# Kernel tuning notes

Measured on AMD Instinct MI355X. Metric: run time of the kernel, lower is better.

## Reference

```python
import jax, jax.numpy as jnp
import numpy as np

I_, J_, D_IN, D_H = 100, 8, 768, 64
N_NODES, N_HE, N_INC, N_CELLS, VOCAB = 160000, 320000, 1600000, 800, 30000
BN_EPS = 1e-5


def setup_inputs() -> dict:
    key = jax.random.key(0)
    ks = jax.random.split(key, 20)
    w = lambda k, s: jax.random.normal(k, s, jnp.float32) * 0.05
    inp = {}
    inp['x'] = jax.random.normal(ks[0], (I_, J_, D_IN), jnp.float32)
    inp['node_tokens'] = jax.random.randint(ks[1], (N_NODES,), 0, VOCAB)
    inp['inc_node'] = jax.random.randint(ks[2], (N_INC,), 0, N_NODES)
    inp['inc_hedge'] = jnp.sort(jax.random.randint(ks[3], (N_INC,), 0, N_HE))
    inp['node2cell'] = jnp.sort(jax.random.randint(ks[4], (N_NODES,), 0, N_CELLS))
    inp['vac_emb'] = w(ks[5], (VOCAB, D_IN))
    inp['fhi_w'] = w(ks[6], (D_IN, D_H)); inp['fhi_b'] = jnp.zeros((D_H,), jnp.float32)
    inp['fin_w'] = w(ks[7], (D_IN, D_H)); inp['fin_b'] = jnp.zeros((D_H,), jnp.float32)
    inp['th1'] = w(ks[8], (D_H, D_H)); inp['b1'] = jnp.zeros((D_H,), jnp.float32)
    inp['th2'] = w(ks[9], (D_H, D_H)); inp['b2'] = jnp.zeros((D_H,), jnp.float32)
    for li, k in zip((1, 2, 3), (ks[10], ks[11], ks[12])):
        inp[f'wc{li}'] = w(k, (D_H, D_H, 3))
        inp[f'bc{li}'] = jnp.zeros((D_H,), jnp.float32)
        inp[f'g{li}'] = jnp.ones((D_H,), jnp.float32)
        inp[f'be{li}'] = jnp.zeros((D_H,), jnp.float32)
        inp[f'm{li}'] = jnp.zeros((D_H,), jnp.float32)
        inp[f'v{li}'] = jnp.ones((D_H,), jnp.float32)
    inp['fct_w'] = w(ks[13], (D_H, D_H)); inp['fct_b'] = jnp.zeros((D_H,), jnp.float32)
    return inp


def _inv_safe(c):
    return jnp.where(c > 0, 1.0 / jnp.maximum(c, 1.0), 0.0)


def _hconv(xf, inc_node, inc_hedge, theta, bias):
    # PyG HypergraphConv (no attention): D^{-1} H W B^{-1} H^T (X Theta) + bias
    xt = xf @ theta                                        # [N, D]
    ones = jnp.ones((inc_node.shape[0],), xt.dtype)
    deg_e = jax.ops.segment_sum(ones, inc_hedge, N_HE)     # B_e
    he = jax.ops.segment_sum(xt[inc_node], inc_hedge, N_HE) * _inv_safe(deg_e)[:, None]
    deg_v = jax.ops.segment_sum(ones, inc_node, N_NODES)   # D_v
    out = jax.ops.segment_sum(he[inc_hedge], inc_node, N_NODES) * _inv_safe(deg_v)[:, None]
    return out + bias


def _conv_bn(h, wc, bc, g, be, m, v):
    # Conv1d(k=3, pad=1) -> ReLU -> BatchNorm1d (inference stats); dropout is eval-mode identity
    h = jax.lax.conv_general_dilated(h, wc, (1,), [(1, 1)],
                                     dimension_numbers=('NCH', 'OIH', 'NCH')) + bc[None, :, None]
    h = jax.nn.relu(h)
    return (h - m[None, :, None]) * (g[None, :, None] / jnp.sqrt(v[None, :, None] + BN_EPS)) + be[None, :, None]


def _forward(x, node_tokens, inc_node, inc_hedge, node2cell, vac_emb, fhi_w, fhi_b,
             fin_w, fin_b, th1, b1, th2, b2, wc1, bc1, g1, be1, m1, v1,
             wc2, bc2, g2, be2, m2, v2, wc3, bc3, g3, be3, m3, v3, fct_w, fct_b):
    # x = fin(x)
    x0 = jnp.einsum('ijd,dh->ijh', x, fin_w) + fin_b       # [100, 8, 64]
    # node_features = fhi(graph_embedding[graph.x])  (gather-dominated)
    nf = vac_emb[node_tokens] @ fhi_w + fhi_b              # [N, 64]
    # two HypergraphConv layers with residuals (eval-mode dropout = identity)
    h1 = jax.nn.relu(_hconv(nf, inc_node, inc_hedge, th1, b1)) + nf
    gx = jax.nn.relu(_hconv(h1, inc_node, inc_hedge, th2, b2)) + nf
    # per-graph mean + max pooling (graph.batch is all-zero per graph => one vector per cell)
    cnt = jax.ops.segment_sum(jnp.ones((N_NODES,), gx.dtype), node2cell, N_CELLS)
    mean_p = jax.ops.segment_sum(gx, node2cell, N_CELLS) * _inv_safe(cnt)[:, None]
    max_p = jax.ops.segment_max(gx, node2cell, N_CELLS)
    max_p = jnp.where(cnt[:, None] > 0, max_p, 0.0)
    cell_emb = 0.5 * (mean_p + max_p)                      # [800, 64]
    x_upd = x0 + 0.3 * cell_emb.reshape(I_, J_, D_H)       # x[i,j] += 0.3*graph_emb
    h = jnp.transpose(x_upd, (0, 2, 1))                    # [100, 64, 8]
    h = _conv_bn(h, wc1, bc1, g1, be1, m1, v1)
    h = _conv_bn(h, wc2, bc2, g2, be2, m2, v2)
    h = _conv_bn(h, wc3, bc3, g3, be3, m3, v3)
    out2 = jnp.mean(h, axis=2) @ fct_w + fct_b             # [100, 64]
    return x_upd, out2


def reference(x, node_tokens, inc_node, inc_hedge, node2cell, vac_emb, fhi_w, fhi_b,
              fin_w, fin_b, th1, b1, th2, b2, wc1, bc1, g1, be1, m1, v1,
              wc2, bc2, g2, be2, m2, v2, wc3, bc3, g3, be3, m3, v3, fct_w, fct_b):
    return _forward(x, node_tokens, inc_node, inc_hedge, node2cell, vac_emb, fhi_w, fhi_b,
                    fin_w, fin_b, th1, b1, th2, b2, wc1, bc1, g1, be1, m1, v1,
                    wc2, bc2, g2, be2, m2, v2, wc3, bc3, g3, be3, m3, v3, fct_w, fct_b)
```

## Files before the change

### kernel.cpp

```cpp
#include <hip/hip_runtime.h>
#include <hip/hip_bf16.h>
#include <cstdint>
#include <cstddef>

#define I_      100
#define J_      8
#define D_IN    768
#define D_H     64
#define N_NODES 160000
#define N_HE    320000
#define N_INC   1600000
#define N_CELLS 800
#define VOCAB   30000

#define NRANGE   256
#define NPR      625
#define EPB      (N_INC / 256)
#define SLAB     8192

typedef unsigned short u16;
using short8 = __attribute__((ext_vector_type(8))) short;
using f32x4  = __attribute__((ext_vector_type(4))) float;

__device__ __forceinline__ float bf2f(u16 u) {
    union { uint32_t i; float f; } x; x.i = ((uint32_t)u) << 16; return x.f;
}
__device__ __forceinline__ u16 f2bf(float f) {
    union { float f; uint32_t i; } x; x.f = f;
    uint32_t b = x.i;
    b += 0x7FFFu + ((b >> 16) & 1u);
    return (u16)(b >> 16);
}
__device__ __forceinline__ float lo_bf(uint32_t u) {
    union { uint32_t i; float f; } x; x.i = u << 16; return x.f;
}
__device__ __forceinline__ float hi_bf(uint32_t u) {
    union { uint32_t i; float f; } x; x.i = u & 0xFFFF0000u; return x.f;
}
__device__ __forceinline__ uint32_t pack_bf2(float a, float b) {
    return (uint32_t)f2bf(a) | ((uint32_t)f2bf(b) << 16);
}

#define G_OFF_HE   (N_INC / 256)
#define G_OFF_CELL (N_NODES / 256)
#define G_CONV_BIG ((D_IN * 64) / 256)
#define G_CONV_SM  ((64 * 64) / 256)
#define G_KA       256
#define G_KB1      256
#define G_KC       256
#define G_KD       256
#define G_PGEMM    ((VOCAB + 63) / 64)
#define G_XT       (N_NODES / 64)
#define G_X0       ((I_ * J_ + 63) / 64)
#define G_HEDGE    (N_HE / 32)
#define G_NODE     (N_NODES / 32)

__device__ __forceinline__ void dev_offsets(int bid, const int* __restrict__ sorted,
                                            int n, int nbins, int* __restrict__ off) {
    int i = bid * 256 + threadIdx.x;
    if (i >= n) return;
    int cur = sorted[i];
    int prev = (i == 0) ? -1 : sorted[i - 1];
    for (int b = prev + 1; b <= cur; ++b) off[b] = i;
    if (i == n - 1) {
        for (int b = cur + 1; b <= nbins; ++b) off[b] = n;
    }
}

__device__ __forceinline__ void dev_convT(int bid, const float* __restrict__ B,
                                          u16* __restrict__ Bt, int K) {
    int g = bid * 256 + threadIdx.x;
    if (g >= K * 64) return;
    int k = g >> 6, n = g & 63;
    Bt[(size_t)n * K + k] = f2bf(B[g]);
}

__device__ __forceinline__ void dev_ka(int bid, const int* __restrict__ inc_node,
                                       int* __restrict__ counts, int* __restrict__ lds) {
    int tid = threadIdx.x;
    lds[tid] = 0;
    __syncthreads();
    int s = bid * EPB, e = s + EPB;
    for (int i = s + tid; i < e; i += 256)
        atomicAdd(&lds[(unsigned)inc_node[i] / NPR], 1);
    __syncthreads();
    counts[bid * NRANGE + tid] = lds[tid];
}

__device__ __forceinline__ void dev_kb1(int r, const int* __restrict__ counts,
                                        int* __restrict__ chunk_off,
                                        int* __restrict__ range_total,
                                        int* __restrict__ lds) {
    int b = threadIdx.x;
    int v = counts[b * NRANGE + r];
    lds[b] = v;
    __syncthreads();
    #pragma unroll
    for (int d = 1; d < 256; d <<= 1) {
        int t = (b >= d) ? lds[b - d] : 0;
        __syncthreads();
        lds[b] += t;
        __syncthreads();
    }
    int incl = lds[b];
    chunk_off[b * NRANGE + r] = incl - v;
    if (b == 255) range_total[r] = incl;
}

__device__ __forceinline__ void dev_kc(int bid, const int* __restrict__ inc_node,
                                       const int* __restrict__ inc_hedge,
                                       const int* __restrict__ chunk_off,
                                       int2* __restrict__ bucket, int* __restrict__ lds) {
    int tid = threadIdx.x;
    int* co  = lds;
    int* cur = lds + 256;
    co[tid]  = tid * SLAB + chunk_off[bid * NRANGE + tid];
    cur[tid] = 0;
    __syncthreads();
    int s = bid * EPB, e = s + EPB;
    for (int i = s + tid; i < e; i += 256) {
        int v = inc_node[i];
        int h = inc_hedge[i];
        int rg = (unsigned)v / NPR;
        int rank = atomicAdd(&cur[rg], 1);
        bucket[co[rg] + rank] = make_int2(v, h);
    }
}

__device__ __forceinline__ void dev_kd(int r, const int2* __restrict__ bucket,
                                       const int* __restrict__ range_total,
                                       int* __restrict__ node_off, int* __restrict__ node_deg,
                                       int* __restrict__ csr, int* __restrict__ lds) {
    int tid = threadIdx.x;
    int* hist = lds;
    int* tsum = lds + 768;
    int* cur  = lds + 1024;
    for (int i = tid; i < 768; i += 256) { hist[i] = 0; cur[i] = 0; }
    __syncthreads();
    int lo = r * NPR;
    int pb = r * SLAB;
    int pe = pb + range_total[r];
    for (int i = pb + tid; i < pe; i += 256)
        atomicAdd(&hist[bucket[i].x - lo], 1);
    __syncthreads();
    int b3 = tid * 3;
    int a0 = hist[b3], a1 = hist[b3 + 1], a2 = hist[b3 + 2];
    int s = a0 + a1 + a2;
    tsum[tid] = s;
    __syncthreads();
    #pragma unroll
    for (int d = 1; d < 256; d <<= 1) {
        int t = (tid >= d) ? tsum[tid - d] : 0;
        __syncthreads();
        tsum[tid] += t;
        __syncthreads();
    }
    int excl = tsum[tid] - s;
    hist[b3]     = excl;
    hist[b3 + 1] = excl + a0;
    hist[b3 + 2] = excl + a0 + a1;
    __syncthreads();
    for (int v = tid; v < NPR; v += 256) {
        int h0 = hist[v];
        node_off[lo + v] = pb + h0;
        node_deg[lo + v] = hist[v + 1] - h0;
    }
    for (int i = pb + tid; i < pe; i += 256) {
        int2 p = bucket[i];
        int l = p.x - lo;
        int k = atomicAdd(&cur[l], 1);
        csr[pb + hist[l] + k] = p.y;
    }
}

template <int BF16_OUT, int GATHER, int KK>
__device__ __forceinline__ void dev_gemm_direct(int wid, const float* __restrict__ A,
                                                const int* __restrict__ tok,
                                                const u16* __restrict__ Bt,
                                                const float* __restrict__ bias,
                                                void* __restrict__ C, int M) {
    int lane = threadIdx.x & 63;
    int m16 = lane & 15, q = lane >> 4;
    int base = wid << 4;
    if (base >= M) return;
    int row = base + m16;
    const float* arow = GATHER ? (A + ((size_t)tok[row] << 6))
                               : (A + (size_t)row * KK);

    f32x4 acc0 = {0.f, 0.f, 0.f, 0.f};
    f32x4 acc1 = {0.f, 0.f, 0.f, 0.f};
    f32x4 acc2 = {0.f, 0.f, 0.f, 0.f};
    f32x4 acc3 = {0.f, 0.f, 0.f, 0.f};

    #pragma unroll 2
    for (int kt = 0; kt < KK; kt += 32) {
        const float* ap = arow + kt + q * 8;
        float4 av0 = *reinterpret_cast<const float4*>(ap);
        float4 av1 = *reinterpret_cast<const float4*>(ap + 4);
        short8 a;
        a[0] = (short)f2bf(av0.x); a[1] = (short)f2bf(av0.y);
        a[2] = (short)f2bf(av0.z); a[3] = (short)f2bf(av0.w);
        a[4] = (short)f2bf(av1.x); a[5] = (short)f2bf(av1.y);
        a[6] = (short)f2bf(av1.z); a[7] = (short)f2bf(av1.w);
        const u16* bp = Bt + (size_t)m16 * KK + kt + q * 8;
        short8 b0 = *reinterpret_cast<const short8*>(bp);
        short8 b1 = *reinterpret_cast<const short8*>(bp + (size_t)16 * KK);
        short8 b2 = *reinterpret_cast<const short8*>(bp + (size_t)32 * KK);
        short8 b3 = *reinterpret_cast<const short8*>(bp + (size_t)48 * KK);
        acc0 = __builtin_amdgcn_mfma_f32_16x16x32_bf16(a, b0, acc0, 0, 0, 0);
        acc1 = __builtin_amdgcn_mfma_f32_16x16x32_bf16(a, b1, acc1, 0, 0, 0);
        acc2 = __builtin_amdgcn_mfma_f32_16x16x32_bf16(a, b2, acc2, 0, 0, 0);
        acc3 = __builtin_amdgcn_mfma_f32_16x16x32_bf16(a, b3, acc3, 0, 0, 0);
    }

    f32x4 accs[4] = {acc0, acc1, acc2, acc3};
    #pragma unroll
    for (int r = 0; r < 4; ++r) {
        int gr = base + q * 4 + r;
        #pragma unroll
        for (int j = 0; j < 4; ++j) {
            int col = j * 16 + m16;
            float v = accs[j][r];
            if (!BF16_OUT) v += bias[col];
            if (BF16_OUT)
                ((u16*)C)[(size_t)gr * 64 + col] = f2bf(v);
            else
                ((float*)C)[(size_t)gr * 64 + col] = v;
        }
    }
}

__device__ __forceinline__ void dev_hedge_sum(int bid, const int* __restrict__ inc_node,
                                              const int* __restrict__ he_off,
                                              const u16* __restrict__ xt,
                                              u16* __restrict__ he) {
    int w = (bid * 256 + (int)threadIdx.x) >> 6;
    int lane = threadIdx.x & 63;
    int sub = lane >> 3;
    int c8 = (lane & 7) << 3;
    int hedge = w * 8 + sub;
    if (hedge >= N_HE) return;
    int s = he_off[hedge], e = he_off[hedge + 1];

    float a0 = 0.f, a1 = 0.f, a2 = 0.f, a3 = 0.f;
    float a4 = 0.f, a5 = 0.f, a6 = 0.f, a7 = 0.f;
    float b0 = 0.f, b1 = 0.f, b2 = 0.f, b3 = 0.f;
    float b4 = 0.f, b5 = 0.f, b6 = 0.f, b7 = 0.f;

    int j = s;
    if ((e - s) & 1) {
        uint4 d = *reinterpret_cast<const uint4*>(xt + (((size_t)inc_node[j]) << 6) + c8);
        a0 += lo_bf(d.x); a1 += hi_bf(d.x);
        a2 += lo_bf(d.y); a3 += hi_bf(d.y);
        a4 += lo_bf(d.z); a5 += hi_bf(d.z);
        a6 += lo_bf(d.w); a7 += hi_bf(d.w);
        ++j;
    }
    int i0 = 0, i1 = 0;
    if (j < e) { i0 = inc_node[j]; i1 = inc_node[j + 1]; }
    for (; j < e; j += 2) {
        int c0 = i0, c1 = i1;
        if (j + 2 < e) { i0 = inc_node[j + 2]; i1 = inc_node[j + 3]; }
        uint4 d0 = *reinterpret_cast<const uint4*>(xt + (((size_t)c0) << 6) + c8);
        uint4 d1 = *reinterpret_cast<const uint4*>(xt + (((size_t)c1) << 6) + c8);
        a0 += lo_bf(d0.x); a1 += hi_bf(d0.x);
        a2 += lo_bf(d0.y); a3 += hi_bf(d0.y);
        a4 += lo_bf(d0.z); a5 += hi_bf(d0.z);
        a6 += lo_bf(d0.w); a7 += hi_bf(d0.w);
        b0 += lo_bf(d1.x); b1 += hi_bf(d1.x);
        b2 += lo_bf(d1.y); b3 += hi_bf(d1.y);
        b4 += lo_bf(d1.z); b5 += hi_bf(d1.z);
        b6 += lo_bf(d1.w); b7 += hi_bf(d1.w);
    }
    a0 += b0; a1 += b1; a2 += b2; a3 += b3;
    a4 += b4; a5 += b5; a6 += b6; a7 += b7;

    float inv = (e > s) ? 1.f / (float)(e - s) : 0.f;
    uint4 o;
    o.x = pack_bf2(a0 * inv, a1 * inv);
    o.y = pack_bf2(a2 * inv, a3 * inv);
    o.z = pack_bf2(a4 * inv, a5 * inv);
    o.w = pack_bf2(a6 * inv, a7 * inv);
    *reinterpret_cast<uint4*>(he + (((size_t)hedge) << 6) + c8) = o;
}

__device__ __forceinline__ void dev_node_sum(int bid, const int* __restrict__ csr,
                                             const int* __restrict__ node_off,
                                             const int* __restrict__ node_deg,
                                             const u16* __restrict__ he,
                                             const float* __restrict__ bias,
                                             const float* __restrict__ P,
                                             const int* __restrict__ tok,
                                             float* __restrict__ out) {
    int w = (bid * 256 + (int)threadIdx.x) >> 6;
    int lane = threadIdx.x & 63;
    int sub = lane >> 3;
    int c8 = (lane & 7) << 3;
    int node = w * 8 + sub;
    if (node >= N_NODES) return;
    int s = node_off[node];
    int e = s + node_deg[node];

    float a0 = 0.f, a1 = 0.f, a2 = 0.f, a3 = 0.f;
    float a4 = 0.f, a5 = 0.f, a6 = 0.f, a7 = 0.f;
    float b0 = 0.f, b1 = 0.f, b2 = 0.f, b3 = 0.f;
    float b4 = 0.f, b5 = 0.f, b6 = 0.f, b7 = 0.f;

    int j = s;
    if ((e - s) & 1) {
        uint4 d = *reinterpret_cast<const uint4*>(he + (((size_t)csr[j]) << 6) + c8);
        a0 += lo_bf(d.x); a1 += hi_bf(d.x);
        a2 += lo_bf(d.y); a3 += hi_bf(d.y);
        a4 += lo_bf(d.z); a5 += hi_bf(d.z);
        a6 += lo_bf(d.w); a7 += hi_bf(d.w);
        ++j;
    }
    int i0 = 0, i1 = 0;
    if (j < e) { i0 = csr[j]; i1 = csr[j + 1]; }
    for (; j < e; j += 2) {
        int c0 = i0, c1 = i1;
        if (j + 2 < e) { i0 = csr[j + 2]; i1 = csr[j + 3]; }
        uint4 d0 = *reinterpret_cast<const uint4*>(he + (((size_t)c0) << 6) + c8);
        uint4 d1 = *reinterpret_cast<const uint4*>(he + (((size_t)c1) << 6) + c8);
        a0 += lo_bf(d0.x); a1 += hi_bf(d0.x);
        a2 += lo_bf(d0.y); a3 += hi_bf(d0.y);
        a4 += lo_bf(d0.z); a5 += hi_bf(d0.z);
        a6 += lo_bf(d0.w); a7 += hi_bf(d0.w);
        b0 += lo_bf(d1.x); b1 += hi_bf(d1.x);
        b2 += lo_bf(d1.y); b3 += hi_bf(d1.y);
        b4 += lo_bf(d1.z); b5 += hi_bf(d1.z);
        b6 += lo_bf(d1.w); b7 += hi_bf(d1.w);
    }
    a0 += b0; a1 += b1; a2 += b2; a3 += b3;
    a4 += b4; a5 += b5; a6 += b6; a7 += b7;

    float inv = (e > s) ? 1.f / (float)(e - s) : 0.f;
    const float* nfp = P + (((size_t)tok[node]) << 6) + c8;
    float4 nv0 = *reinterpret_cast<const float4*>(nfp);
    float4 nv1 = *reinterpret_cast<const float4*>(nfp + 4);
    float4 o0, o1;
    o0.x = fmaxf(fmaf(a0, inv, bias[c8 + 0]), 0.f) + nv0.x;
    o0.y = fmaxf(fmaf(a1, inv, bias[c8 + 1]), 0.f) + nv0.y;
    o0.z = fmaxf(fmaf(a2, inv, bias[c8 + 2]), 0.f) + nv0.z;
    o0.w = fmaxf(fmaf(a3, inv, bias[c8 + 3]), 0.f) + nv0.w;
    o1.x = fmaxf(fmaf(a4, inv, bias[c8 + 4]), 0.f) + nv1.x;
    o1.y = fmaxf(fmaf(a5, inv, bias[c8 + 5]), 0.f) + nv1.y;
    o1.z = fmaxf(fmaf(a6, inv, bias[c8 + 6]), 0.f) + nv1.z;
    o1.w = fmaxf(fmaf(a7, inv, bias[c8 + 7]), 0.f) + nv1.w;
    float* op = out + (((size_t)node) << 6) + c8;
    *reinterpret_cast<float4*>(op) = o0;
    *reinterpret_cast<float4*>(op + 4) = o1;
}

__global__ __launch_bounds__(256) void k_p0(const float* __restrict__ fhi_w,
                                            const float* __restrict__ fin_w,
                                            const float* __restrict__ th1,
                                            const float* __restrict__ th2,
                                            u16* __restrict__ Bt_fhi, u16* __restrict__ Bt_fin,
                                            u16* __restrict__ Bt_th1, u16* __restrict__ Bt_th2,
                                            const int* __restrict__ inc_node,
                                            int* __restrict__ counts) {
    __shared__ int lds[256];
    int bid = blockIdx.x;
    if (bid < G_KA) { dev_ka(bid, inc_node, counts, lds); return; }
    bid -= G_KA;
    if (bid < G_CONV_BIG) { dev_convT(bid, fhi_w, Bt_fhi, D_IN); return; }
    bid -= G_CONV_BIG;
    if (bid < G_CONV_BIG) { dev_convT(bid, fin_w, Bt_fin, D_IN); return; }
    bid -= G_CONV_BIG;
    if (bid < G_CONV_SM) { dev_convT(bid, th1, Bt_th1, 64); return; }
    bid -= G_CONV_SM;
    dev_convT(bid, th2, Bt_th2, 64);
}

__global__ __launch_bounds__(256) void k_p1(const float* __restrict__ vac_emb,
                                            const u16* __restrict__ Bt_fhi,
                                            const float* __restrict__ fhi_b, float* __restrict__ P,
                                            const int* __restrict__ counts,
                                            int* __restrict__ chunk_off, int* __restrict__ range_total,
                                            const int* __restrict__ inc_hedge,
                                            const int* __restrict__ node2cell,
                                            int* __restrict__ he_off, int* __restrict__ cell_off) {
    __shared__ int lds[256];
    int bid = blockIdx.x;
    if (bid < G_PGEMM) {
        int wid = bid * 4 + ((int)threadIdx.x >> 6);
        dev_gemm_direct<0, 0, D_IN>(wid, vac_emb, nullptr, Bt_fhi, fhi_b, P, VOCAB);
        return;
    }
    bid -= G_PGEMM;
    if (bid < G_KB1) { dev_kb1(bid, counts, chunk_off, range_total, lds); return; }
    bid -= G_KB1;
    if (bid < G_OFF_HE) { dev_offsets(bid, inc_hedge, N_INC, N_HE, he_off); return; }
    bid -= G_OFF_HE;
    dev_offsets(bid, node2cell, N_NODES, N_CELLS, cell_off);
}

__global__ __launch_bounds__(256) void k_p2(const float* __restrict__ P,
                                            const int* __restrict__ tok,
                                            const u16* __restrict__ Bt_th1, u16* __restrict__ xt,
                                            const float* __restrict__ x, const u16* __restrict__ Bt_fin,
                                            const float* __restrict__ fin_b, float* __restrict__ x0,
                                            const int* __restrict__ inc_node,
                                            const int* __restrict__ inc_hedge,
                                            const int* __restrict__ chunk_off,
                                            int2* __restrict__ bucket) {
    __shared__ int lds[512];
    int bid = blockIdx.x;
    if (bid < G_XT) {
        int wid = bid * 4 + ((int)threadIdx.x >> 6);
        dev_gemm_direct<1, 1, 64>(wid, P, tok, Bt_th1, nullptr, xt, N_NODES);
        return;
    }
    bid -= G_XT;
    if (bid < G_KC) { dev_kc(bid, inc_node, inc_hedge, chunk_off, bucket, lds); return; }
    bid -= G_KC;
    {
        int wid = bid * 4 + ((int)threadIdx.x >> 6);
        dev_gemm_direct<0, 0, D_IN>(wid, x, nullptr, Bt_fin, fin_b, x0, I_ * J_);
    }
}

__global__ __launch_bounds__(256) void k_p3(const int* __restrict__ inc_node,
                                            const int* __restrict__ he_off,
                                            const u16* __restrict__ xt, u16* __restrict__ he,
                                            const int2* __restrict__ bucket,
                                            const int* __restrict__ range_total,
                                            int* __restrict__ node_off, int* __restrict__ node_deg,
                                            int* __restrict__ csr) {
    __shared__ int lds[1792];
    int bid = blockIdx.x;
    if (bid < G_HEDGE) { dev_hedge_sum(bid, inc_node, he_off, xt, he); return; }
    bid -= G_HEDGE;
    dev_kd(bid, bucket, range_total, node_off, node_deg, csr, lds);
}

__global__ __launch_bounds__(256) void k_xt2(const float* __restrict__ A,
                                             const u16* __restrict__ Bt,
                                             u16* __restrict__ xt) {
    int wid = blockIdx.x * 4 + ((int)threadIdx.x >> 6);
    dev_gemm_direct<1, 0, 64>(wid, A, nullptr, Bt, nullptr, xt, N_NODES);
}

__global__ __launch_bounds__(256) void k_hedge_sum(const int* __restrict__ inc_node,
                                                   const int* __restrict__ he_off,
                                                   const u16* __restrict__ xt,
                                                   u16* __restrict__ he) {
    dev_hedge_sum(blockIdx.x, inc_node, he_off, xt, he);
}

__global__ __launch_bounds__(256) void k_node_sum(const int* __restrict__ csr,
                                                  const int* __restrict__ node_off,
                                                  const int* __restrict__ node_deg,
                                                  const u16* __restrict__ he,
                                                  const float* __restrict__ bias,
                                                  const float* __restrict__ P,
                                                  const int* __restrict__ tok,
                                                  float* __restrict__ out) {
    dev_node_sum(blockIdx.x, csr, node_off, node_deg, he, bias, P, tok, out);
}

__global__ __launch_bounds__(256) void k_pool(const float* __restrict__ gx,
                                              const int* __restrict__ cell_off,
                                              const float* __restrict__ x0,
                                              float* __restrict__ out1) {
    __shared__ float ssum[4][64];
    __shared__ float smax[4][64];
    int c = blockIdx.x;
    int lane = threadIdx.x & 63;
    int w = threadIdx.x >> 6;
    int s = cell_off[c], e = cell_off[c + 1];
    float sum = 0.f, mx = -INFINITY;
    for (int n = s + w; n < e; n += 4) {
        float v = gx[((size_t)n << 6) + lane];
        sum += v;
        mx = fmaxf(mx, v);
    }
    ssum[w][lane] = sum;
    smax[w][lane] = mx;
    __syncthreads();
    if (w == 0) {
        sum = ssum[0][lane] + ssum[1][lane] + ssum[2][lane] + ssum[3][lane];
        mx = fmaxf(fmaxf(smax[0][lane], smax[1][lane]), fmaxf(smax[2][lane], smax[3][lane]));
        int cnt = e - s;
        float mean = (cnt > 0) ? sum / (float)cnt : 0.f;
        float mp = (cnt > 0) ? mx : 0.f;
        float ce = 0.5f * (mean + mp);
        out1[((size_t)c << 6) + lane] = x0[((size_t)c << 6) + lane] + 0.3f * ce;
    }
}

__global__ __launch_bounds__(256) void k_tcn(
    const float* __restrict__ xu,
    const float* __restrict__ wc1, const float* __restrict__ bc1, const float* __restrict__ g1,
    const float* __restrict__ be1, const float* __restrict__ m1, const float* __restrict__ v1,
    const float* __restrict__ wc2, const float* __restrict__ bc2, const float* __restrict__ g2,
    const float* __restrict__ be2, const float* __restrict__ m2, const float* __restrict__ v2,
    const float* __restrict__ wc3, const float* __restrict__ bc3, const float* __restrict__ g3,
    const float* __restrict__ be3, const float* __restrict__ m3, const float* __restrict__ v3,
    const float* __restrict__ fct_w, const float* __restrict__ fct_b,
    float* __restrict__ out2) {
    __shared__ float w_lds[64 * 64 * 3];
    __shared__ float hA[64][10];
    __shared__ float hB[64][10];
    __shared__ float mo[64];

    int n = blockIdx.x, tid = threadIdx.x;

    if (tid < 64) {
        hA[tid][0] = 0.f; hA[tid][9] = 0.f;
        hB[tid][0] = 0.f; hB[tid][9] = 0.f;
    }
    #pragma unroll
    for (int l = tid; l < 512; l += 256) {
        int t = l >> 6, i = l & 63;
        hA[i][t + 1] = xu[(size_t)n * 512 + l];
    }

    const float* wcs[3] = {wc1, wc2, wc3};
    const float* bcs[3] = {bc1, bc2, bc3};
    const float* gs[3]  = {g1, g2, g3};
    const float* bes[3] = {be1, be2, be3};
    const float* ms[3]  = {m1, m2, m3};
    const float* vs[3]  = {v1, v2, v3};

    float (*hin)[10] = hA;
    float (*hout)[10] = hB;

    #pragma unroll
    for (int li = 0; li < 3; ++li) {
        for (int l = tid; l < 64 * 64 * 3; l += 256) w_lds[l] = wcs[li][l];
        __syncthreads();
        #pragma unroll
        for (int rep = 0; rep < 2; ++rep) {
            int idx = tid + rep * 256;
            int o = idx >> 3, t = idx & 7;
            float acc = bcs[li][o];
            #pragma unroll 8
            for (int i = 0; i < 64; ++i) {
                const float* wr = &w_lds[o * 192 + i * 3];
                acc = fmaf(hin[i][t + 0], wr[0], acc);
                acc = fmaf(hin[i][t + 1], wr[1], acc);
                acc = fmaf(hin[i][t + 2], wr[2], acc);
            }
            acc = fmaxf(acc, 0.f);
            float sc = gs[li][o] * rsqrtf(vs[li][o] + 1e-5f);
            acc = (acc - ms[li][o]) * sc + bes[li][o];
            hout[o][t + 1] = acc;
        }
        __syncthreads();
        float (*tmp)[10] = hin; hin = hout; hout = tmp;
    }

    if (tid < 64) {
        float s = 0.f;
        #pragma unroll
        for (int t = 0; t < 8; ++t) s += hin[tid][t + 1];
        mo[tid] = s * 0.125f;
    }
    __syncthreads();
    if (tid < 64) {
        float acc = fct_b[tid];
        #pragma unroll 8
        for (int o = 0; o < 64; ++o) acc = fmaf(mo[o], fct_w[o * 64 + tid], acc);
        out2[(size_t)n * 64 + tid] = acc;
    }
}

extern "C" void kernel_launch(void* const* d_in, const int* in_sizes, int n_in,
                              void* d_out, int out_size, void* d_ws, size_t ws_size,
                              hipStream_t stream) {
    (void)in_sizes; (void)n_in; (void)out_size; (void)ws_size;

    const float* x          = (const float*)d_in[0];
    const int*   node_tok   = (const int*)d_in[1];
    const int*   inc_node   = (const int*)d_in[2];
    const int*   inc_hedge  = (const int*)d_in[3];
    const int*   node2cell  = (const int*)d_in[4];
    const float* vac_emb    = (const float*)d_in[5];
    const float* fhi_w      = (const float*)d_in[6];
    const float* fhi_b      = (const float*)d_in[7];
    const float* fin_w      = (const float*)d_in[8];
    const float* fin_b      = (const float*)d_in[9];
    const float* th1        = (const float*)d_in[10];
    const float* b1         = (const float*)d_in[11];
    const float* th2        = (const float*)d_in[12];
    const float* b2         = (const float*)d_in[13];
    const float* fct_w      = (const float*)d_in[32];
    const float* fct_b      = (const float*)d_in[33];

    char* ws = (char*)d_ws;
    size_t off = 0;
    float* P        = (float*)(ws + off); off += (size_t)VOCAB * 64 * 4;
    float* hbuf     = (float*)(ws + off); off += (size_t)N_NODES * 64 * 4;
    u16*   xt       = (u16*)(ws + off);   off += (size_t)N_NODES * 64 * 2;
    u16*   he       = (u16*)(ws + off);   off += (size_t)N_HE * 64 * 2;
    int2*  bucket   = (int2*)(ws + off);  off += (size_t)NRANGE * SLAB * 8;
    int*   csr      = (int*)(ws + off);   off += (size_t)NRANGE * SLAB * 4;
    float* x0       = (float*)(ws + off); off += (size_t)N_CELLS * 64 * 4;
    u16*   Bt_fhi   = (u16*)(ws + off);   off += (size_t)64 * D_IN * 2;
    u16*   Bt_fin   = (u16*)(ws + off);   off += (size_t)64 * D_IN * 2;
    u16*   Bt_th1   = (u16*)(ws + off);   off += (size_t)64 * 64 * 2;
    u16*   Bt_th2   = (u16*)(ws + off);   off += (size_t)64 * 64 * 2;
    int*   he_off   = (int*)(ws + off);   off += ((size_t)(N_HE + 1) * 4 + 255) / 256 * 256;
    int*   node_off = (int*)(ws + off);   off += (size_t)N_NODES * 4;
    int*   node_deg = (int*)(ws + off);   off += (size_t)N_NODES * 4;
    int*   cell_off = (int*)(ws + off);   off += ((size_t)(N_CELLS + 1) * 4 + 255) / 256 * 256;

    int*  counts      = (int*)hbuf;
    int*  chunk_off   = counts + NRANGE * NRANGE;
    int*  range_total = chunk_off + NRANGE * NRANGE;

    float* out1 = (float*)d_out;
    float* out2 = out1 + (size_t)I_ * J_ * D_H;

    k_p0<<<G_KA + 2 * G_CONV_BIG + 2 * G_CONV_SM, 256, 0, stream>>>(
        fhi_w, fin_w, th1, th2, Bt_fhi, Bt_fin, Bt_th1, Bt_th2, inc_node, counts);

    k_p1<<<G_PGEMM + G_KB1 + G_OFF_HE + G_OFF_CELL, 256, 0, stream>>>(
        vac_emb, Bt_fhi, fhi_b, P, counts, chunk_off, range_total,
        inc_hedge, node2cell, he_off, cell_off);

    k_p2<<<G_XT + G_KC + G_X0, 256, 0, stream>>>(P, node_tok, Bt_th1, xt,
                                                 x, Bt_fin, fin_b, x0,
                                                 inc_node, inc_hedge, chunk_off, bucket);

    k_p3<<<G_HEDGE + G_KD, 256, 0, stream>>>(inc_node, he_off, xt, he,
                                             bucket, range_total, node_off, node_deg, csr);

    k_node_sum<<<G_NODE, 256, 0, stream>>>(csr, node_off, node_deg, he, b1, P, node_tok, hbuf);

    k_xt2<<<G_XT, 256, 0, stream>>>(hbuf, Bt_th2, xt);

    k_hedge_sum<<<G_HEDGE, 256, 0, stream>>>(inc_node, he_off, xt, he);

    k_node_sum<<<G_NODE, 256, 0, stream>>>(csr, node_off, node_deg, he, b2, P, node_tok, hbuf);

    k_pool<<<N_CELLS, 256, 0, stream>>>(hbuf, cell_off, x0, out1);

    k_tcn<<<I_, 256, 0, stream>>>(out1,
        (const float*)d_in[14], (const float*)d_in[15], (const float*)d_in[16],
        (const float*)d_in[17], (const float*)d_in[18], (const float*)d_in[19],
        (const float*)d_in[20], (const float*)d_in[21], (const float*)d_in[22],
        (const float*)d_in[23], (const float*)d_in[24], (const float*)d_in[25],
        (const float*)d_in[26], (const float*)d_in[27], (const float*)d_in[28],
        (const float*)d_in[29], (const float*)d_in[30], (const float*)d_in[31],
        fct_w, fct_b, out2);
}
```

Before: 514.7 us.

## Build node CSR with global atomics instead of two-pass range bucketing

Replaces the four-stage range-bucketed counting sort (per-chunk LDS histograms, cross-chunk scan, bucket scatter, per-range local sort) with direct global atomic degree counting, a per-range scan to produce node offsets, and an atomic-cursor scatter straight into the CSR. This removes the intermediate int2 bucket buffer and one full pass over the incidences. In exchange it relies on contended global atomics over random node indices and adds zeroing of two node-sized arrays. Within-node edge order becomes nondeterministic, which can change float summation order.

```diff
diff --git a/kernel.cpp b/kernel.cpp
--- a/kernel.cpp
+++ b/kernel.cpp
@@ -15,7 +15,6 @@
 
 #define NRANGE   256
 #define NPR      625
-#define EPB      (N_INC / 256)
 #define SLAB     8192
 
 typedef unsigned short u16;
@@ -45,10 +44,10 @@
 #define G_OFF_CELL (N_NODES / 256)
 #define G_CONV_BIG ((D_IN * 64) / 256)
 #define G_CONV_SM  ((64 * 64) / 256)
-#define G_KA       256
-#define G_KB1      256
-#define G_KC       256
-#define G_KD       256
+#define G_ZD4      ((N_NODES / 4 + 255) / 256)
+#define G_KAH      512
+#define G_KBS      256
+#define G_KCS      512
 #define G_PGEMM    ((VOCAB + 63) / 64)
 #define G_XT       (N_NODES / 64)
 #define G_X0       ((I_ * J_ + 63) / 64)
@@ -75,101 +74,54 @@
     Bt[(size_t)n * K + k] = f2bf(B[g]);
 }
 
-__device__ __forceinline__ void dev_ka(int bid, const int* __restrict__ inc_node,
-                                       int* __restrict__ counts, int* __restrict__ lds) {
+__device__ __forceinline__ void dev_zero4(int bid, int* __restrict__ p, int n4) {
+    int g = bid * 256 + threadIdx.x;
+    if (g < n4) reinterpret_cast<int4*>(p)[g] = make_int4(0, 0, 0, 0);
+}
+
+__device__ __forceinline__ void dev_kah(int bid, const int* __restrict__ inc_node,
+                                        int* __restrict__ node_deg) {
+    int s = bid * (N_INC / G_KAH);
+    int e = s + (N_INC / G_KAH);
+    for (int i = s + (int)threadIdx.x; i < e; i += 256)
+        atomicAdd(&node_deg[inc_node[i]], 1);
+}
+
+__device__ __forceinline__ void dev_kbs(int r, const int* __restrict__ node_deg,
+                                        int* __restrict__ node_off, int* __restrict__ lds) {
     int tid = threadIdx.x;
-    lds[tid] = 0;
-    __syncthreads();
-    int s = bid * EPB, e = s + EPB;
-    for (int i = s + tid; i < e; i += 256)
-        atomicAdd(&lds[(unsigned)inc_node[i] / NPR], 1);
-    __syncthreads();
-    counts[bid * NRANGE + tid] = lds[tid];
-}
-
-__device__ __forceinline__ void dev_kb1(int r, const int* __restrict__ counts,
-                                        int* __restrict__ chunk_off,
-                                        int* __restrict__ range_total,
-                                        int* __restrict__ lds) {
-    int b = threadIdx.x;
-    int v = counts[b * NRANGE + r];
-    lds[b] = v;
+    int lo = r * NPR, pb = r * SLAB;
+    int v0 = tid * 3;
+    int d0 = (v0     < NPR) ? node_deg[lo + v0]     : 0;
+    int d1 = (v0 + 1 < NPR) ? node_deg[lo + v0 + 1] : 0;
+    int d2 = (v0 + 2 < NPR) ? node_deg[lo + v0 + 2] : 0;
+    int s = d0 + d1 + d2;
+    lds[tid] = s;
     __syncthreads();
     #pragma unroll
     for (int d = 1; d < 256; d <<= 1) {
-        int t = (b >= d) ? lds[b - d] : 0;
+        int t = (tid >= d) ? lds[tid - d] : 0;
         __syncthreads();
-        lds[b] += t;
+        lds[tid] += t;
         __syncthreads();
     }
-    int incl = lds[b];
-    chunk_off[b * NRANGE + r] = incl - v;
-    if (b == 255) range_total[r] = incl;
-}
-
-__device__ __forceinline__ void dev_kc(int bid, const int* __restrict__ inc_node,
-                                       const int* __restrict__ inc_hedge,
-                                       const int* __restrict__ chunk_off,
-                                       int2* __restrict__ bucket, int* __restrict__ lds) {
-    int tid = threadIdx.x;
-    int* co  = lds;
-    int* cur = lds + 256;
-    co[tid]  = tid * SLAB + chunk_off[bid * NRANGE + tid];
-    cur[tid] = 0;
-    __syncthreads();
-    int s = bid * EPB, e = s + EPB;
-    for (int i = s + tid; i < e; i += 256) {
+    int excl = lds[tid] - s;
+    if (v0     < NPR) node_off[lo + v0]     = pb + excl;
+    if (v0 + 1 < NPR) node_off[lo + v0 + 1] = pb + excl + d0;
+    if (v0 + 2 < NPR) node_off[lo + v0 + 2] = pb + excl + d0 + d1;
+}
+
+__device__ __forceinline__ void dev_kcs(int bid, const int* __restrict__ inc_node,
+                                        const int* __restrict__ inc_hedge,
+                                        const int* __restrict__ node_off,
+                                        int* __restrict__ cur, int* __restrict__ csr) {
+    int s = bid * (N_INC / G_KCS);
+    int e = s + (N_INC / G_KCS);
+    for (int i = s + (int)threadIdx.x; i < e; i += 256) {
         int v = inc_node[i];
         int h = inc_hedge[i];
-        int rg = (unsigned)v / NPR;
-        int rank = atomicAdd(&cur[rg], 1);
-        bucket[co[rg] + rank] = make_int2(v, h);
-    }
-}
-
-__device__ __forceinline__ void dev_kd(int r, const int2* __restrict__ bucket,
-                                       const int* __restrict__ range_total,
-                                       int* __restrict__ node_off, int* __restrict__ node_deg,
-                                       int* __restrict__ csr, int* __restrict__ lds) {
-    int tid = threadIdx.x;
-    int* hist = lds;
-    int* tsum = lds + 768;
-    int* cur  = lds + 1024;
-    for (int i = tid; i < 768; i += 256) { hist[i] = 0; cur[i] = 0; }
-    __syncthreads();
-    int lo = r * NPR;
-    int pb = r * SLAB;
-    int pe = pb + range_total[r];
-    for (int i = pb + tid; i < pe; i += 256)
-        atomicAdd(&hist[bucket[i].x - lo], 1);
-    __syncthreads();
-    int b3 = tid * 3;
-    int a0 = hist[b3], a1 = hist[b3 + 1], a2 = hist[b3 + 2];
-    int s = a0 + a1 + a2;
-    tsum[tid] = s;
-    __syncthreads();
-    #pragma unroll
-    for (int d = 1; d < 256; d <<= 1) {
-        int t = (tid >= d) ? tsum[tid - d] : 0;
-        __syncthreads();
-        tsum[tid] += t;
-        __syncthreads();
-    }
-    int excl = tsum[tid] - s;
-    hist[b3]     = excl;
-    hist[b3 + 1] = excl + a0;
-    hist[b3 + 2] = excl + a0 + a1;
-    __syncthreads();
-    for (int v = tid; v < NPR; v += 256) {
-        int h0 = hist[v];
-        node_off[lo + v] = pb + h0;
-        node_deg[lo + v] = hist[v + 1] - h0;
-    }
-    for (int i = pb + tid; i < pe; i += 256) {
-        int2 p = bucket[i];
-        int l = p.x - lo;
-        int k = atomicAdd(&cur[l], 1);
-        csr[pb + hist[l] + k] = p.y;
+        int k = atomicAdd(&cur[v], 1);
+        csr[node_off[v] + k] = h;
     }
 }
 
@@ -358,12 +310,12 @@
                                             const float* __restrict__ th2,
                                             u16* __restrict__ Bt_fhi, u16* __restrict__ Bt_fin,
                                             u16* __restrict__ Bt_th1, u16* __restrict__ Bt_th2,
-                                            const int* __restrict__ inc_node,
-                                            int* __restrict__ counts) {
-    __shared__ int lds[256];
+                                            int* __restrict__ node_deg, int* __restrict__ cur) {
     int bid = blockIdx.x;
-    if (bid < G_KA) { dev_ka(bid, inc_node, counts, lds); return; }
-    bid -= G_KA;
+    if (bid < G_ZD4) { dev_zero4(bid, node_deg, N_NODES / 4); return; }
+    bid -= G_ZD4;
+    if (bid < G_ZD4) { dev_zero4(bid, cur, N_NODES / 4); return; }
+    bid -= G_ZD4;
     if (bid < G_CONV_BIG) { dev_convT(bid, fhi_w, Bt_fhi, D_IN); return; }
     bid -= G_CONV_BIG;
     if (bid < G_CONV_BIG) { dev_convT(bid, fin_w, Bt_fin, D_IN); return; }
@@ -376,12 +328,11 @@
 __global__ __launch_bounds__(256) void k_p1(const float* __restrict__ vac_emb,
                                             const u16* __restrict__ Bt_fhi,
                                             const float* __restrict__ fhi_b, float* __restrict__ P,
-                                            const int* __restrict__ counts,
-                                            int* __restrict__ chunk_off, int* __restrict__ range_total,
+                                            const int* __restrict__ inc_node,
+                                            int* __restrict__ node_deg,
                                             const int* __restrict__ inc_hedge,
                                             const int* __restrict__ node2cell,
                                             int* __restrict__ he_off, int* __restrict__ cell_off) {
-    __shared__ int lds[256];
     int bid = blockIdx.x;
     if (bid < G_PGEMM) {
         int wid = bid * 4 + ((int)threadIdx.x >> 6);
@@ -389,8 +340,8 @@
         return;
     }
     bid -= G_PGEMM;
-    if (bid < G_KB1) { dev_kb1(bid, counts, chunk_off, range_total, lds); return; }
-    bid -= G_KB1;
+    if (bid < G_KAH) { dev_kah(bid, inc_node, node_deg); return; }
+    bid -= G_KAH;
     if (bid < G_OFF_HE) { dev_offsets(bid, inc_hedge, N_INC, N_HE, he_off); return; }
     bid -= G_OFF_HE;
     dev_offsets(bid, node2cell, N_NODES, N_CELLS, cell_off);
@@ -401,20 +352,18 @@
                                             const u16* __restrict__ Bt_th1, u16* __restrict__ xt,
                                             const float* __restrict__ x, const u16* __restrict__ Bt_fin,
                                             const float* __restrict__ fin_b, float* __restrict__ x0,
-                                            const int* __restrict__ inc_node,
-                                            const int* __restrict__ inc_hedge,
-                                            const int* __restrict__ chunk_off,
-                                            int2* __restrict__ bucket) {
-    __shared__ int lds[512];
+                                            const int* __restrict__ node_deg,
+                                            int* __restrict__ node_off) {
+    __shared__ int lds[256];
     int bid = blockIdx.x;
+    if (bid < G_KBS) { dev_kbs(bid, node_deg, node_off, lds); return; }
+    bid -= G_KBS;
     if (bid < G_XT) {
         int wid = bid * 4 + ((int)threadIdx.x >> 6);
         dev_gemm_direct<1, 1, 64>(wid, P, tok, Bt_th1, nullptr, xt, N_NODES);
         return;
     }
     bid -= G_XT;
-    if (bid < G_KC) { dev_kc(bid, inc_node, inc_hedge, chunk_off, bucket, lds); return; }
-    bid -= G_KC;
     {
         int wid = bid * 4 + ((int)threadIdx.x >> 6);
         dev_gemm_direct<0, 0, D_IN>(wid, x, nullptr, Bt_fin, fin_b, x0, I_ * J_);
@@ -424,15 +373,13 @@
 __global__ __launch_bounds__(256) void k_p3(const int* __restrict__ inc_node,
                                             const int* __restrict__ he_off,
                                             const u16* __restrict__ xt, u16* __restrict__ he,
-                                            const int2* __restrict__ bucket,
-                                            const int* __restrict__ range_total,
-                                            int* __restrict__ node_off, int* __restrict__ node_deg,
-                                            int* __restrict__ csr) {
-    __shared__ int lds[1792];
+                                            const int* __restrict__ inc_hedge,
+                                            const int* __restrict__ node_off,
+                                            int* __restrict__ cur, int* __restrict__ csr) {
     int bid = blockIdx.x;
-    if (bid < G_HEDGE) { dev_hedge_sum(bid, inc_node, he_off, xt, he); return; }
-    bid -= G_HEDGE;
-    dev_kd(bid, bucket, range_total, node_off, node_deg, csr, lds);
+    if (bid < G_KCS) { dev_kcs(bid, inc_node, inc_hedge, node_off, cur, csr); return; }
+    bid -= G_KCS;
+    dev_hedge_sum(bid, inc_node, he_off, xt, he);
 }
 
 __global__ __launch_bounds__(256) void k_xt2(const float* __restrict__ A,
@@ -595,7 +542,6 @@
     float* hbuf     = (float*)(ws + off); off += (size_t)N_NODES * 64 * 4;
     u16*   xt       = (u16*)(ws + off);   off += (size_t)N_NODES * 64 * 2;
     u16*   he       = (u16*)(ws + off);   off += (size_t)N_HE * 64 * 2;
-    int2*  bucket   = (int2*)(ws + off);  off += (size_t)NRANGE * SLAB * 8;
     int*   csr      = (int*)(ws + off);   off += (size_t)NRANGE * SLAB * 4;
     float* x0       = (float*)(ws + off); off += (size_t)N_CELLS * 64 * 4;
     u16*   Bt_fhi   = (u16*)(ws + off);   off += (size_t)64 * D_IN * 2;
@@ -605,28 +551,25 @@
     int*   he_off   = (int*)(ws + off);   off += ((size_t)(N_HE + 1) * 4 + 255) / 256 * 256;
     int*   node_off = (int*)(ws + off);   off += (size_t)N_NODES * 4;
     int*   node_deg = (int*)(ws + off);   off += (size_t)N_NODES * 4;
+    int*   cur      = (int*)(ws + off);   off += (size_t)N_NODES * 4;
     int*   cell_off = (int*)(ws + off);   off += ((size_t)(N_CELLS + 1) * 4 + 255) / 256 * 256;
-
-    int*  counts      = (int*)hbuf;
-    int*  chunk_off   = counts + NRANGE * NRANGE;
-    int*  range_total = chunk_off + NRANGE * NRANGE;
 
     float* out1 = (float*)d_out;
     float* out2 = out1 + (size_t)I_ * J_ * D_H;
 
-    k_p0<<<G_KA + 2 * G_CONV_BIG + 2 * G_CONV_SM, 256, 0, stream>>>(
-        fhi_w, fin_w, th1, th2, Bt_fhi, Bt_fin, Bt_th1, Bt_th2, inc_node, counts);
-
-    k_p1<<<G_PGEMM + G_KB1 + G_OFF_HE + G_OFF_CELL, 256, 0, stream>>>(
-        vac_emb, Bt_fhi, fhi_b, P, counts, chunk_off, range_total,
+    k_p0<<<2 * G_ZD4 + 2 * G_CONV_BIG + 2 * G_CONV_SM, 256, 0, stream>>>(
+        fhi_w, fin_w, th1, th2, Bt_fhi, Bt_fin, Bt_th1, Bt_th2, node_deg, cur);
+
+    k_p1<<<G_PGEMM + G_KAH + G_OFF_HE + G_OFF_CELL, 256, 0, stream>>>(
+        vac_emb, Bt_fhi, fhi_b, P, inc_node, node_deg,
         inc_hedge, node2cell, he_off, cell_off);
 
-    k_p2<<<G_XT + G_KC + G_X0, 256, 0, stream>>>(P, node_tok, Bt_th1, xt,
-                                                 x, Bt_fin, fin_b, x0,
-                                                 inc_node, inc_hedge, chunk_off, bucket);
-
-    k_p3<<<G_HEDGE + G_KD, 256, 0, stream>>>(inc_node, he_off, xt, he,
-                                             bucket, range_total, node_off, node_deg, csr);
+    k_p2<<<G_KBS + G_XT + G_X0, 256, 0, stream>>>(P, node_tok, Bt_th1, xt,
+                                                  x, Bt_fin, fin_b, x0,
+                                                  node_deg, node_off);
+
+    k_p3<<<G_KCS + G_HEDGE, 256, 0, stream>>>(inc_node, he_off, xt, he,
+                                              inc_hedge, node_off, cur, csr);
 
     k_node_sum<<<G_NODE, 256, 0, stream>>>(csr, node_off, node_deg, he, b1, P, node_tok, hbuf);
 
```

New measurement: 593.9 us. 1.15x slower.

## Split incidence counting/scatter into more chunks and schedule long-tail blocks first

Applied to the files above, without the earlier changes.

Raises the number of incidence chunks used by the range histogram and bucket-scatter phases from 256 to 1000. The per-range scan now handles four chunks per thread so that 1000 chunk offsets can be computed. In the fused kernels, block order is changed so the long-running histogram-scan, scatter and CSR-build blocks are dispatched before the GEMM and hedge-sum blocks. The aim is more parallelism and less tail latency in the serial scatter phases, at the cost of a larger counts array and a little more scan work.

```diff
diff --git a/kernel.cpp b/kernel.cpp
--- a/kernel.cpp
+++ b/kernel.cpp
@@ -15,8 +15,9 @@
 
 #define NRANGE   256
 #define NPR      625
-#define EPB      (N_INC / 256)
 #define SLAB     8192
+#define NCHUNK   1000
+#define EPB      (N_INC / NCHUNK)
 
 typedef unsigned short u16;
 using short8 = __attribute__((ext_vector_type(8))) short;
@@ -45,9 +46,9 @@
 #define G_OFF_CELL (N_NODES / 256)
 #define G_CONV_BIG ((D_IN * 64) / 256)
 #define G_CONV_SM  ((64 * 64) / 256)
-#define G_KA       256
+#define G_KA       NCHUNK
 #define G_KB1      256
-#define G_KC       256
+#define G_KC       NCHUNK
 #define G_KD       256
 #define G_PGEMM    ((VOCAB + 63) / 64)
 #define G_XT       (N_NODES / 64)
@@ -91,20 +92,28 @@
                                         int* __restrict__ chunk_off,
                                         int* __restrict__ range_total,
                                         int* __restrict__ lds) {
-    int b = threadIdx.x;
-    int v = counts[b * NRANGE + r];
-    lds[b] = v;
+    int tid = threadIdx.x;
+    int c0 = tid * 4;
+    int v0 = (c0     < NCHUNK) ? counts[(c0    ) * NRANGE + r] : 0;
+    int v1 = (c0 + 1 < NCHUNK) ? counts[(c0 + 1) * NRANGE + r] : 0;
+    int v2 = (c0 + 2 < NCHUNK) ? counts[(c0 + 2) * NRANGE + r] : 0;
+    int v3 = (c0 + 3 < NCHUNK) ? counts[(c0 + 3) * NRANGE + r] : 0;
+    int s = v0 + v1 + v2 + v3;
+    lds[tid] = s;
     __syncthreads();
     #pragma unroll
     for (int d = 1; d < 256; d <<= 1) {
-        int t = (b >= d) ? lds[b - d] : 0;
+        int t = (tid >= d) ? lds[tid - d] : 0;
         __syncthreads();
-        lds[b] += t;
+        lds[tid] += t;
         __syncthreads();
     }
-    int incl = lds[b];
-    chunk_off[b * NRANGE + r] = incl - v;
-    if (b == 255) range_total[r] = incl;
+    int run = lds[tid] - s;
+    if (c0     < NCHUNK) { chunk_off[(c0    ) * NRANGE + r] = run; run += v0; }
+    if (c0 + 1 < NCHUNK) { chunk_off[(c0 + 1) * NRANGE + r] = run; run += v1; }
+    if (c0 + 2 < NCHUNK) { chunk_off[(c0 + 2) * NRANGE + r] = run; run += v2; }
+    if (c0 + 3 < NCHUNK) { chunk_off[(c0 + 3) * NRANGE + r] = run; run += v3; }
+    if (tid == 255) range_total[r] = lds[255];
 }
 
 __device__ __forceinline__ void dev_kc(int bid, const int* __restrict__ inc_node,
@@ -383,14 +392,14 @@
                                             int* __restrict__ he_off, int* __restrict__ cell_off) {
     __shared__ int lds[256];
     int bid = blockIdx.x;
+    if (bid < G_KB1) { dev_kb1(bid, counts, chunk_off, range_total, lds); return; }
+    bid -= G_KB1;
     if (bid < G_PGEMM) {
         int wid = bid * 4 + ((int)threadIdx.x >> 6);
         dev_gemm_direct<0, 0, D_IN>(wid, vac_emb, nullptr, Bt_fhi, fhi_b, P, VOCAB);
         return;
     }
     bid -= G_PGEMM;
-    if (bid < G_KB1) { dev_kb1(bid, counts, chunk_off, range_total, lds); return; }
-    bid -= G_KB1;
     if (bid < G_OFF_HE) { dev_offsets(bid, inc_hedge, N_INC, N_HE, he_off); return; }
     bid -= G_OFF_HE;
     dev_offsets(bid, node2cell, N_NODES, N_CELLS, cell_off);
@@ -407,14 +416,14 @@
                                             int2* __restrict__ bucket) {
     __shared__ int lds[512];
     int bid = blockIdx.x;
+    if (bid < G_KC) { dev_kc(bid, inc_node, inc_hedge, chunk_off, bucket, lds); return; }
+    bid -= G_KC;
     if (bid < G_XT) {
         int wid = bid * 4 + ((int)threadIdx.x >> 6);
         dev_gemm_direct<1, 1, 64>(wid, P, tok, Bt_th1, nullptr, xt, N_NODES);
         return;
     }
     bid -= G_XT;
-    if (bid < G_KC) { dev_kc(bid, inc_node, inc_hedge, chunk_off, bucket, lds); return; }
-    bid -= G_KC;
     {
         int wid = bid * 4 + ((int)threadIdx.x >> 6);
         dev_gemm_direct<0, 0, D_IN>(wid, x, nullptr, Bt_fin, fin_b, x0, I_ * J_);
@@ -430,9 +439,9 @@
                                             int* __restrict__ csr) {
     __shared__ int lds[1792];
     int bid = blockIdx.x;
-    if (bid < G_HEDGE) { dev_hedge_sum(bid, inc_node, he_off, xt, he); return; }
-    bid -= G_HEDGE;
-    dev_kd(bid, bucket, range_total, node_off, node_deg, csr, lds);
+    if (bid < G_KD) { dev_kd(bid, bucket, range_total, node_off, node_deg, csr, lds); return; }
+    bid -= G_KD;
+    dev_hedge_sum(bid, inc_node, he_off, xt, he);
 }
 
 __global__ __launch_bounds__(256) void k_xt2(const float* __restrict__ A,
@@ -608,24 +617,25 @@
     int*   cell_off = (int*)(ws + off);   off += ((size_t)(N_CELLS + 1) * 4 + 255) / 256 * 256;
 
     int*  counts      = (int*)hbuf;
-    int*  chunk_off   = counts + NRANGE * NRANGE;
-    int*  range_total = chunk_off + NRANGE * NRANGE;
+    int*  chunk_off   = counts + NCHUNK * NRANGE;
+    int*  range_total = chunk_off + NCHUNK * NRANGE;
 
     float* out1 = (float*)d_out;
     float* out2 = out1 + (size_t)I_ * J_ * D_H;
 
     k_p0<<<G_KA + 2 * G_CONV_BIG + 2 * G_CONV_SM, 256, 0, stream>>>(
-        fhi_w, fin_w, th1, th2, Bt_fhi, Bt_fin, Bt_th1, Bt_th2, inc_node, counts);
-
-    k_p1<<<G_PGEMM + G_KB1 + G_OFF_HE + G_OFF_CELL, 256, 0, stream>>>(
+        fhi_w, fin_w, th1, th2, Bt_fhi, Bt_fin, Bt_th1, Bt_th2,
+        inc_node, counts);
+
+    k_p1<<<G_KB1 + G_PGEMM + G_OFF_HE + G_OFF_CELL, 256, 0, stream>>>(
         vac_emb, Bt_fhi, fhi_b, P, counts, chunk_off, range_total,
         inc_hedge, node2cell, he_off, cell_off);
 
-    k_p2<<<G_XT + G_KC + G_X0, 256, 0, stream>>>(P, node_tok, Bt_th1, xt,
-                                                 x, Bt_fin, fin_b, x0,
-                                                 inc_node, inc_hedge, chunk_off, bucket);
-
-    k_p3<<<G_HEDGE + G_KD, 256, 0, stream>>>(inc_node, he_off, xt, he,
+    k_p2<<<G_KC + G_XT + G_X0, 256, 0, stream>>>(
+        P, node_tok, Bt_th1, xt, x, Bt_fin, fin_b, x0,
+        inc_node, inc_hedge, chunk_off, bucket);
+
+    k_p3<<<G_KD + G_HEDGE, 256, 0, stream>>>(inc_node, he_off, xt, he,
                                              bucket, range_total, node_off, node_deg, csr);
 
     k_node_sum<<<G_NODE, 256, 0, stream>>>(csr, node_off, node_deg, he, b1, P, node_tok, hbuf);
```

Measured after the change: 502.8 us. 1.02x faster.
